# Kernel tuning notes

Measured on AMD Instinct MI355X. Metric: run time of the kernel, lower is better.

Reference implementation:

```python
import jax, jax.numpy as jnp
import numpy as np


def setup_inputs() -> dict:
    key = jax.random.key(0)
    k1, k2, k3 = jax.random.split(key, 3)
    N, K, C, M = 16, 32768, 16, 128
    pred_boxes = jax.random.normal(k1, (N, K, 5), dtype=jnp.float32)
    pred_cls = jax.random.normal(k2, (N, K, C), dtype=jnp.float32)
    target = jax.random.uniform(k3, (N, M, 5), dtype=jnp.float32)
    return {"pred_boxes": pred_boxes, "pred_cls": pred_cls, "target": target}


def _losses(pred_boxes, pred_cls, target):
    N, K, _ = pred_boxes.shape
    M = target.shape[1]
    C = pred_cls.shape[2]
    mask = target.sum(axis=2) != 0                      # (N, M)
    maskf = mask.astype(pred_boxes.dtype)
    denom = maskf.sum()
    tboxes = target[..., 1:]                            # (N, M, 4) corners (x1,y1,x2,y2)
    tcls = target[..., 0].astype(jnp.int32)             # (N, M)
    pconf = pred_boxes[..., 4]                          # (N, K)
    pb = pred_boxes[..., :4]                            # (N, K, 4) (x, y, w, h)

    # pred corners (N, 1, K)
    p_x1 = pb[:, None, :, 0]
    p_y1 = pb[:, None, :, 1]
    p_x2 = (pb[..., 2] + pb[..., 0])[:, None, :]
    p_y2 = (pb[..., 3] + pb[..., 1])[:, None, :]
    # target corners (N, M, 1)
    t_x1 = tboxes[..., 0:1]
    t_y1 = tboxes[..., 1:2]
    t_x2 = tboxes[..., 2:3]
    t_y2 = tboxes[..., 3:4]

    ix1 = jnp.maximum(p_x1, t_x1)
    iy1 = jnp.maximum(p_y1, t_y1)
    ix2 = jnp.minimum(p_x2, t_x2)
    iy2 = jnp.minimum(p_y2, t_y2)
    inter = jnp.clip(ix2 - ix1 + 1, 0) * jnp.clip(iy2 - iy1 + 1, 0)   # (N, M, K)
    a1 = (p_x2 - p_x1 + 1) * (p_y2 - p_y1 + 1)
    a2 = (t_x2 - t_x1 + 1) * (t_y2 - t_y1 + 1)
    iou = inter / (a1 + a2 - inter + 1e-16)

    best = jnp.argmax(iou, axis=-1)                     # (N, M)
    best_idx = jnp.where(mask, best, 0)                 # masked targets keep index 0 (as torch init)

    best_pb = jnp.take_along_axis(pb, best_idx[..., None], axis=1)       # (N, M, 4)
    best_cls = jnp.take_along_axis(pred_cls, best_idx[..., None], axis=1)  # (N, M, C)
    # NOTE: faithful to original: conf gather indices are never updated -> always index 0
    conf_idx = jnp.zeros((N, M), dtype=jnp.int32)
    best_conf = jax.nn.sigmoid(jnp.take_along_axis(pconf, conf_idx, axis=1))  # (N, M)

    def masked_mean(v):
        return (v * maskf).sum() / denom

    logp = jax.nn.log_softmax(best_cls, axis=-1)
    ce = -jnp.take_along_axis(logp, tcls[..., None], axis=-1)[..., 0]
    loss_cls = masked_mean(ce)

    loss_x = masked_mean((best_pb[..., 0] - tboxes[..., 0]) ** 2)
    loss_y = masked_mean((best_pb[..., 1] - tboxes[..., 1]) ** 2)
    loss_w = masked_mean((best_pb[..., 2] - (tboxes[..., 2] - tboxes[..., 0])) ** 2)
    loss_h = masked_mean((best_pb[..., 3] - (tboxes[..., 3] - tboxes[..., 1])) ** 2)

    labels = (best_conf > 0.5).astype(best_conf.dtype)
    bce = -(labels * jnp.log(best_conf) + (1.0 - labels) * jnp.log(1.0 - best_conf))
    loss_conf = masked_mean(bce)

    loss = loss_cls + loss_x + loss_y + loss_w + loss_h + loss_conf
    return loss, loss_cls, loss_x, loss_y, loss_w, loss_h, loss_conf


def reference(pred_boxes, pred_cls, target):
    return _losses(pred_boxes, pred_cls, target)
```

## Files before the change

### kernel.cpp

```cpp
#include <hip/hip_runtime.h>
#include <hip/hip_bf16.h>
#include <math.h>

constexpr int N_ = 16;
constexpr int K_ = 32768;
constexpr int C_ = 16;
constexpr int M_ = 128;

constexpr int KC = 256;
constexpr int CHUNKS = K_ / KC;
constexpr int WAVES = 4;
constexpr int KSL = KC / WAVES;

#define POISON_I ((int)0xAAAAAAAAu)

__device__ __forceinline__ void store_agent_u64(unsigned long long* p,
                                                unsigned long long v) {
  __hip_atomic_store(p, v, __ATOMIC_RELAXED, __HIP_MEMORY_SCOPE_AGENT);
}
__device__ __forceinline__ unsigned long long load_agent_u64(
    const unsigned long long* p) {
  return __hip_atomic_load(p, __ATOMIC_RELAXED, __HIP_MEMORY_SCOPE_AGENT);
}
__device__ __forceinline__ void store_agent_f32(float* p, float v) {
  __hip_atomic_store(p, v, __ATOMIC_RELAXED, __HIP_MEMORY_SCOPE_AGENT);
}
__device__ __forceinline__ float load_agent_f32(const float* p) {
  return __hip_atomic_load(p, __ATOMIC_RELAXED, __HIP_MEMORY_SCOPE_AGENT);
}

__global__ __launch_bounds__(256, 8) void fused_loss_kernel(
    const float* __restrict__ pred_boxes,
    const float* __restrict__ pred_cls,
    const float* __restrict__ target,
    unsigned long long* __restrict__ pair,
    float* __restrict__ ws2,
    int* __restrict__ cnt,
    float* __restrict__ out) {
  __shared__ float4 lds4[KC];
  __shared__ float piou_s[WAVES][M_];
  __shared__ int pidx_s[WAVES][M_];
  __shared__ float miou[M_];
  __shared__ int midx[M_];
  __shared__ float red[4][7];
  __shared__ int s_flag;

  const int chunk = blockIdx.x;
  const int n = blockIdx.y;
  const int k0 = chunk * KC;
  const int tid = threadIdx.x;

  {
    const float* p = pred_boxes + ((size_t)(n * K_ + k0 + tid)) * 5;
    const float x = p[0];
    const float y = p[1];
    const float bw = p[2];
    const float bh = p[3];
    const float px2 = bw + x;
    const float py2 = bh + y;
    lds4[tid] = make_float4(x, y, px2 + 1.0f, py2 + 1.0f);
  }
  __syncthreads();

  const int wv = tid >> 6;
  const int lane = tid & 63;
  const int m0 = lane;
  const int m1 = lane + 64;

  const float* tgA = target + ((size_t)(n * M_ + m0)) * 5;
  const float tx1A = tgA[1];
  const float ty1A = tgA[2];
  const float tx2A = tgA[3] + 1.0f;
  const float ty2A = tgA[4] + 1.0f;
  const float a2A = (tgA[3] - tgA[1] + 1.0f) * (tgA[4] - tgA[2] + 1.0f) + 1e-16f;

  const float* tgB = target + ((size_t)(n * M_ + m1)) * 5;
  const float tx1B = tgB[1];
  const float ty1B = tgB[2];
  const float tx2B = tgB[3] + 1.0f;
  const float ty2B = tgB[4] + 1.0f;
  const float a2B = (tgB[3] - tgB[1] + 1.0f) * (tgB[4] - tgB[2] + 1.0f) + 1e-16f;

  float bestA = -INFINITY, bestB = -INFINITY;
  int bkA = 0, bkB = 0;

  const int ks = wv * KSL;
  const int ke = ks + KSL;
#pragma unroll 4
  for (int kl = ks; kl < ke; ++kl) {
    const float4 v = lds4[kl];
    const float a1 = (v.z - v.x) * (v.w - v.y);
    {
      float ww = fminf(v.z, tx2A) - fmaxf(v.x, tx1A);
      float hh = fminf(v.w, ty2A) - fmaxf(v.y, ty1A);
      ww = fmaxf(ww, 0.0f);
      hh = fmaxf(hh, 0.0f);
      const float inter = ww * hh;
      const float iou = inter * __builtin_amdgcn_rcpf((a1 + a2A) - inter);
      const bool gt = iou > bestA;
      bestA = gt ? iou : bestA;
      bkA = gt ? kl : bkA;
    }
    {
      float ww = fminf(v.z, tx2B) - fmaxf(v.x, tx1B);
      float hh = fminf(v.w, ty2B) - fmaxf(v.y, ty1B);
      ww = fmaxf(ww, 0.0f);
      hh = fmaxf(hh, 0.0f);
      const float inter = ww * hh;
      const float iou = inter * __builtin_amdgcn_rcpf((a1 + a2B) - inter);
      const bool gt = iou > bestB;
      bestB = gt ? iou : bestB;
      bkB = gt ? kl : bkB;
    }
  }

  piou_s[wv][m0] = bestA;
  pidx_s[wv][m0] = bkA;
  piou_s[wv][m1] = bestB;
  pidx_s[wv][m1] = bkB;
  __syncthreads();

  if (tid < M_) {
    float b = piou_s[0][tid];
    int bi = pidx_s[0][tid];
#pragma unroll
    for (int w2 = 1; w2 < WAVES; ++w2) {
      const float v = piou_s[w2][tid];
      const int id = pidx_s[w2][tid];
      const bool gt = v > b;
      b = gt ? v : b;
      bi = gt ? id : bi;
    }
    store_agent_u64(&pair[((size_t)n * CHUNKS + chunk) * M_ + tid],
                    ((unsigned long long)__float_as_uint(b) << 32) |
                        (unsigned)(k0 + bi));
  }

  __syncthreads();
  if (tid == 0) {
    const int old = atomicAdd(&cnt[n], 1);
    s_flag = (old == POISON_I + (CHUNKS - 1)) || (old == CHUNKS - 1);
  }
  __syncthreads();
  if (!s_flag) return;

  {
    const int m = tid & (M_ - 1);
    const int half = tid >> 7;
    float b2 = -INFINITY;
    int i2 = 0;
    const unsigned long long* pp = pair + ((size_t)n * CHUNKS) * M_ + m;
    const int cs = half * (CHUNKS / 2);
    const int ce = cs + (CHUNKS / 2);
#pragma unroll 8
    for (int c = cs; c < ce; ++c) {
      const unsigned long long pk = load_agent_u64(&pp[(size_t)c * M_]);
      const float v = __uint_as_float((unsigned)(pk >> 32));
      const int id = (int)(unsigned)pk;
      const bool gt = v > b2;
      b2 = gt ? v : b2;
      i2 = gt ? id : i2;
    }
    if (half == 1) {
      miou[m] = b2;
      midx[m] = i2;
    }
    __syncthreads();

    float acc[7] = {0, 0, 0, 0, 0, 0, 0};
    if (half == 0) {
      const float o = miou[m];
      const int oi = midx[m];
      const bool gt = o > b2;
      const int bidx0 = gt ? oi : i2;

      const float* tg2 = target + ((size_t)(n * M_ + m)) * 5;
      const float t0 = tg2[0], t1 = tg2[1], t2 = tg2[2], t3 = tg2[3],
                  t4 = tg2[4];
      const float sum5 = t0 + t1 + t2 + t3 + t4;
      const float mk = (sum5 != 0.0f) ? 1.0f : 0.0f;
      const int bidx = (sum5 != 0.0f) ? bidx0 : 0;

      const float* pb = pred_boxes + ((size_t)(n * K_ + bidx)) * 5;
      const float b0 = pb[0], b1 = pb[1], bw = pb[2], bh = pb[3];

      const float4* pc =
          (const float4*)(pred_cls + ((size_t)(n * K_ + bidx)) * C_);
      float vals[C_];
#pragma unroll
      for (int q = 0; q < 4; ++q) {
        const float4 vv = pc[q];
        vals[q * 4 + 0] = vv.x;
        vals[q * 4 + 1] = vv.y;
        vals[q * 4 + 2] = vv.z;
        vals[q * 4 + 3] = vv.w;
      }
      int tcls = (int)t0;
      tcls = tcls < 0 ? 0 : (tcls >= C_ ? C_ - 1 : tcls);
      float mx = -INFINITY;
#pragma unroll
      for (int q = 0; q < C_; ++q) mx = fmaxf(mx, vals[q]);
      float se = 0.0f;
#pragma unroll
      for (int q = 0; q < C_; ++q) se += expf(vals[q] - mx);
      const float ce2 = logf(se) + mx - vals[tcls];

      const float dx = b0 - t1;
      const float dy = b1 - t2;
      const float dw = bw - (t3 - t1);
      const float dh = bh - (t4 - t2);

      const float pcf = pred_boxes[(size_t)n * K_ * 5 + 4];
      const float bc = 1.0f / (1.0f + expf(-pcf));
      const float bce = (bc > 0.5f) ? -logf(bc) : -logf(1.0f - bc);

      acc[0] = mk;
      acc[1] = mk * ce2;
      acc[2] = mk * dx * dx;
      acc[3] = mk * dy * dy;
      acc[4] = mk * dw * dw;
      acc[5] = mk * dh * dh;
      acc[6] = mk * bce;
    }

#pragma unroll
    for (int i = 0; i < 7; ++i) {
      float v = acc[i];
      for (int off = 32; off > 0; off >>= 1) v += __shfl_down(v, off, 64);
      acc[i] = v;
    }
    const int lane2 = tid & 63;
    const int wid = tid >> 6;
    if (lane2 == 0) {
#pragma unroll
      for (int i = 0; i < 7; ++i) red[wid][i] = acc[i];
    }
    __syncthreads();

    if (tid == 0) {
#pragma unroll
      for (int i = 0; i < 7; ++i)
        store_agent_f32(&ws2[n * 8 + i],
                        red[0][i] + red[1][i] + red[2][i] + red[3][i]);
    }
    __syncthreads();
    if (tid == 0) {
      const int old2 = atomicAdd(&cnt[N_], 1);
      s_flag = (old2 == POISON_I + (N_ - 1)) || (old2 == N_ - 1);
    }
    __syncthreads();
  }

  if (s_flag && tid == 0) {
    float s[7] = {0, 0, 0, 0, 0, 0, 0};
    for (int nn = 0; nn < N_; ++nn)
#pragma unroll
      for (int i = 0; i < 7; ++i) s[i] += load_agent_f32(&ws2[nn * 8 + i]);
    const float denom = s[0];
    const float lc = s[1] / denom;
    const float lx = s[2] / denom;
    const float ly = s[3] / denom;
    const float lw = s[4] / denom;
    const float lh = s[5] / denom;
    const float lf = s[6] / denom;
    out[0] = lc + lx + ly + lw + lh + lf;
    out[1] = lc;
    out[2] = lx;
    out[3] = ly;
    out[4] = lw;
    out[5] = lh;
    out[6] = lf;
  }
}

extern "C" void kernel_launch(void* const* d_in, const int* in_sizes, int n_in,
                              void* d_out, int out_size, void* d_ws, size_t ws_size,
                              hipStream_t stream) {
  const float* pred_boxes = (const float*)d_in[0];
  const float* pred_cls = (const float*)d_in[1];
  const float* target = (const float*)d_in[2];
  float* out = (float*)d_out;

  unsigned long long* pair = (unsigned long long*)d_ws;
  float* ws2 = (float*)(pair + (size_t)N_ * CHUNKS * M_);
  int* cnt = (int*)(ws2 + N_ * 8);

  dim3 g(CHUNKS, N_);
  fused_loss_kernel<<<g, 256, 0, stream>>>(pred_boxes, pred_cls, target,
                                           pair, ws2, cnt, out);
}
```

Before: 126.4 us.

## Replace per-chunk argmax partials with 64-bit atomicMin on packed IoU keys

```diff
diff --git a/kernel.cpp b/kernel.cpp
--- a/kernel.cpp
+++ b/kernel.cpp
@@ -14,10 +14,6 @@
 
 #define POISON_I ((int)0xAAAAAAAAu)
 
-__device__ __forceinline__ void store_agent_u64(unsigned long long* p,
-                                                unsigned long long v) {
-  __hip_atomic_store(p, v, __ATOMIC_RELAXED, __HIP_MEMORY_SCOPE_AGENT);
-}
 __device__ __forceinline__ unsigned long long load_agent_u64(
     const unsigned long long* p) {
   return __hip_atomic_load(p, __ATOMIC_RELAXED, __HIP_MEMORY_SCOPE_AGENT);
@@ -33,15 +29,13 @@
     const float* __restrict__ pred_boxes,
     const float* __restrict__ pred_cls,
     const float* __restrict__ target,
-    unsigned long long* __restrict__ pair,
+    unsigned long long* __restrict__ rowmin,
     float* __restrict__ ws2,
     int* __restrict__ cnt,
     float* __restrict__ out) {
   __shared__ float4 lds4[KC];
   __shared__ float piou_s[WAVES][M_];
   __shared__ int pidx_s[WAVES][M_];
-  __shared__ float miou[M_];
-  __shared__ int midx[M_];
   __shared__ float red[4][7];
   __shared__ int s_flag;
 
@@ -131,9 +125,11 @@
       b = gt ? v : b;
       bi = gt ? id : bi;
     }
-    store_agent_u64(&pair[((size_t)n * CHUNKS + chunk) * M_ + tid],
-                    ((unsigned long long)__float_as_uint(b) << 32) |
-                        (unsigned)(k0 + bi));
+    const unsigned kb = __float_as_uint(b);
+    const unsigned ord = kb ^ (unsigned)(((int)kb >> 31) | 0x80000000);
+    const unsigned long long ikey =
+        ((unsigned long long)(~ord) << 32) | (unsigned)(k0 + bi);
+    atomicMin(&rowmin[(size_t)n * M_ + tid], ikey);
   }
 
   __syncthreads();
@@ -146,33 +142,11 @@
 
   {
     const int m = tid & (M_ - 1);
-    const int half = tid >> 7;
-    float b2 = -INFINITY;
-    int i2 = 0;
-    const unsigned long long* pp = pair + ((size_t)n * CHUNKS) * M_ + m;
-    const int cs = half * (CHUNKS / 2);
-    const int ce = cs + (CHUNKS / 2);
-#pragma unroll 8
-    for (int c = cs; c < ce; ++c) {
-      const unsigned long long pk = load_agent_u64(&pp[(size_t)c * M_]);
-      const float v = __uint_as_float((unsigned)(pk >> 32));
-      const int id = (int)(unsigned)pk;
-      const bool gt = v > b2;
-      b2 = gt ? v : b2;
-      i2 = gt ? id : i2;
-    }
-    if (half == 1) {
-      miou[m] = b2;
-      midx[m] = i2;
-    }
-    __syncthreads();
-
     float acc[7] = {0, 0, 0, 0, 0, 0, 0};
-    if (half == 0) {
-      const float o = miou[m];
-      const int oi = midx[m];
-      const bool gt = o > b2;
-      const int bidx0 = gt ? oi : i2;
+    if (tid < M_) {
+      const unsigned long long pk =
+          load_agent_u64(&rowmin[(size_t)n * M_ + m]);
+      const int bidx0 = (int)(unsigned)pk;
 
       const float* tg2 = target + ((size_t)(n * M_ + m)) * 5;
       const float t0 = tg2[0], t1 = tg2[1], t2 = tg2[2], t3 = tg2[3],
@@ -281,11 +255,11 @@
   const float* target = (const float*)d_in[2];
   float* out = (float*)d_out;
 
-  unsigned long long* pair = (unsigned long long*)d_ws;
-  float* ws2 = (float*)(pair + (size_t)N_ * CHUNKS * M_);
+  unsigned long long* rowmin = (unsigned long long*)d_ws;
+  float* ws2 = (float*)(rowmin + (size_t)N_ * M_);
   int* cnt = (int*)(ws2 + N_ * 8);
 
   dim3 g(CHUNKS, N_);
   fused_loss_kernel<<<g, 256, 0, stream>>>(pred_boxes, pred_cls, target,
-                                           pair, ws2, cnt, out);
-}
+                                           rowmin, ws2, cnt, out);
+}
```

Measured after the change: 120.3 us. -4.8%, faster.
